# Optimization experiments

Hardware: AMD Instinct MI355X
Metric: run time of the kernel (lower is better)

The kernel has to match this reference:

```python
import jax, jax.numpy as jnp
import numpy as np

C1 = 0.01 ** 2
C2 = 0.03 ** 2
IN_CH = 3
WIN = 11
LEVELS = 5


def _gauss_kernel(k=WIN, sigma=1.5, c=IN_CH):
    ax = np.arange(k, dtype=np.float32) - (k - 1) / 2.0
    g = np.exp(-(ax ** 2) / (2.0 * sigma ** 2))
    g = g / g.sum()
    w2d = np.outer(g, g).astype(np.float32)  # [k,k]
    return jnp.asarray(np.tile(w2d[None, None], (c, 1, 1, 1)))  # [C,1,k,k]


def _dwconv(x, w):
    # depthwise (grouped) conv, 'same' padding for odd kernel
    pad = (w.shape[-1] - 1) // 2
    return jax.lax.conv_general_dilated(
        x, w, window_strides=(1, 1), padding=[(pad, pad), (pad, pad)],
        feature_group_count=x.shape[1],
        dimension_numbers=("NCHW", "OIHW", "NCHW"))


def _ssim_loss(i1, i2, w):
    m1 = _dwconv(i1, w)
    m2 = _dwconv(i2, w)
    m1sq = m1 * m1
    m2sq = m2 * m2
    m12 = m1 * m2
    s1 = _dwconv(i1 * i1, w) - m1sq
    s2 = _dwconv(i2 * i2, w) - m2sq
    s12 = _dwconv(i1 * i2, w) - m12
    ssim = (2 * m12 + C1) * (2 * s12 + C2) / ((m1sq + m2sq + C1) * (s1 + s2 + C2))
    return 1.0 - ssim.mean()


def _avg_pool2(x):
    B, C, H, W = x.shape
    return x.reshape(B, C, H // 2, 2, W // 2, 2).mean(axis=(3, 5))


def setup_inputs() -> dict:
    key = jax.random.key(0)
    k1, k2 = jax.random.split(key)
    img1 = jax.random.uniform(k1, (16, IN_CH, 512, 512), dtype=jnp.float32)
    img2 = jax.random.uniform(k2, (16, IN_CH, 512, 512), dtype=jnp.float32)
    inp = {"img1": img1, "img2": img2}
    for i in range(LEVELS):
        inp[f"g{i}"] = _gauss_kernel()
    return inp


def reference(img1, img2, g0, g1, g2, g3, g4):
    loss = jnp.asarray(0.0, dtype=img1.dtype)
    for w in (g0, g1, g2, g3, g4):
        loss = loss + _ssim_loss(img1, img2, w)
        img1 = _avg_pool2(img1)
        img2 = _avg_pool2(img2)
    return loss
```

## Files before the change

kernel.cpp:

```cpp
#include <hip/hip_runtime.h>
#include <math.h>

#define WIN 11
#define PAD 5
#define TW 64
#define TH 64

struct GW { float g[WIN]; };

template<bool EMIT>
__device__ __forceinline__ float ssim_wave_tile(
    const float* __restrict__ p1, const float* __restrict__ p2,
    int W, int X0, int Y0, const GW& gw, float2* __restrict__ rb,
    float* __restrict__ o1a, float* __restrict__ o1b, int Wout)
{
    const int lane = threadIdx.x & 63;
    const int gx = X0 + lane;
    const bool cval = gx < W;
    const int hx   = (lane < 5) ? (X0 - 5 + lane) : (X0 + 59 + lane);
    const bool hval = (lane < 10) && ((unsigned)hx < (unsigned)W);
    const int hpos = (lane < 5) ? lane : (64 + lane);
    const int cpos = 5 + lane;

    float vMp[11], vSp[11], vMq[11], vSq[11];
#pragma unroll
    for (int k = 0; k < 11; ++k) { vMp[k] = 0.f; vSp[k] = 0.f; vMq[k] = 0.f; vSq[k] = 0.f; }

    float part = 0.f;
    float pprev = 0.f, qprev = 0.f;
    float a, b, ah, bh;

    auto LOAD = [&](int t, float& oa, float& ob, float& oah, float& obh) {
        int y = Y0 - PAD + t;
        oa = 0.f; ob = 0.f; oah = 0.f; obh = 0.f;
        if ((unsigned)y < (unsigned)W) {
            const float* r1 = p1 + (size_t)y * W;
            const float* r2 = p2 + (size_t)y * W;
            if (cval) { oa  = r1[gx]; ob  = r2[gx]; }
            if (hval) { oah = r1[hx]; obh = r2[hx]; }
        }
    };

    LOAD(0, a, b, ah, bh);

#pragma unroll 2
    for (int t = 0; t < 74; ++t) {
        float na, nb, nah, nbh;
        LOAD(t + 1, na, nb, nah, nbh);

        float p = a + b, q = a - b;
        float ph = ah + bh, qh = ah - bh;
        rb[cpos] = make_float2(p, q);
        if (lane < 10) rb[hpos] = make_float2(ph, qh);
        __builtin_amdgcn_wave_barrier();

        float hp = 0.f, hq = 0.f, hpp = 0.f, hqq = 0.f;
#pragma unroll
        for (int j = 0; j < WIN; ++j) {
            float2 v = rb[lane + j];
            float g = gw.g[j];
            hp  = fmaf(g, v.x, hp);
            hpp = fmaf(g, v.x * v.x, hpp);
            hq  = fmaf(g, v.y, hq);
            hqq = fmaf(g, v.y * v.y, hqq);
        }
        __builtin_amdgcn_wave_barrier();

#pragma unroll
        for (int k = 0; k < 11; ++k) {
            float g = gw.g[10 - k];
            vMp[k] = fmaf(g, hp,  vMp[k]);
            vSp[k] = fmaf(g, hpp, vSp[k]);
            vMq[k] = fmaf(g, hq,  vMq[k]);
            vSq[k] = fmaf(g, hqq, vSq[k]);
        }

        if (EMIT) {
            if (t >= 6 && t <= 68 && (t & 1) == 0) {
                float sp_ = p + pprev, sq_ = q + qprev;
                float sp2 = sp_ + __shfl_down(sp_, 1, 64);
                float sq2 = sq_ + __shfl_down(sq_, 1, 64);
                if ((lane & 1) == 0) {
                    float P = sp2 * 0.25f, Q = sq2 * 0.25f;
                    int yo = (t - 6) >> 1;
                    size_t oo = (size_t)((Y0 >> 1) + yo) * Wout + ((X0 >> 1) + (lane >> 1));
                    o1a[oo] = (P + Q) * 0.5f;
                    o1b[oo] = (P - Q) * 0.5f;
                }
            }
            pprev = p; qprev = q;
        }

        if (t >= 10) {
            int o = t - 10;
            bool yok = (unsigned)(Y0 + o) < (unsigned)W;
            float Mp = vMp[0], Sp_ = vSp[0], Mq = vMq[0], Sq_ = vSq[0];
            const float C1v = 1e-4f, C2v = 9e-4f;
            float A = Mp * Mp, B = Mq * Mq;
            float ABp = A + B, ABm = A - B;
            float SSp = Sp_ + Sq_, SSm = Sp_ - Sq_;
            float n1 = fmaf(0.5f, ABm, C1v);
            float n2 = fmaf(0.5f, SSm - ABm, C2v);
            float e1 = fmaf(0.5f, ABp, C1v);
            float e2 = fmaf(0.5f, SSp - ABp, C2v);
            float v = (n1 * n2) * __builtin_amdgcn_rcpf(e1 * e2);
            part += (cval && yok) ? v : 0.f;
        }

#pragma unroll
        for (int k = 0; k < 10; ++k) {
            vMp[k] = vMp[k + 1]; vSp[k] = vSp[k + 1];
            vMq[k] = vMq[k + 1]; vSq[k] = vSq[k + 1];
        }
        vMp[10] = 0.f; vSp[10] = 0.f; vMq[10] = 0.f; vSq[10] = 0.f;

        a = na; b = nb; ah = nah; bh = nbh;
    }

    return part;
}

__global__ __launch_bounds__(256, 4) void ssim_l0_kernel(
    const float* __restrict__ i1, const float* __restrict__ i2,
    float* __restrict__ a1, float* __restrict__ b1,
    double* __restrict__ acc, GW gw)
{
    __shared__ float2 rbs[4][80];
    const int wid = threadIdx.x >> 6;
    const int w = blockIdx.x * 4 + wid;
    const int img = w >> 6;
    const int tt = w & 63;
    const int tx = tt & 7, ty = tt >> 3;
    const size_t off  = (size_t)img * 512 * 512;
    const size_t ooff = (size_t)img * 256 * 256;

    float part = ssim_wave_tile<true>(i1 + off, i2 + off, 512, tx * TW, ty * TH,
                                      gw, rbs[wid], a1 + ooff, b1 + ooff, 256);
#pragma unroll
    for (int o = 32; o > 0; o >>= 1) part += __shfl_down(part, o, 64);
    if ((threadIdx.x & 63) == 0) atomicAdd(acc, (double)part);
}

__global__ __launch_bounds__(256, 4) void ssim_rest_kernel(
    const float* __restrict__ a1, const float* __restrict__ b1,
    const float* __restrict__ a2, const float* __restrict__ b2,
    const float* __restrict__ a3, const float* __restrict__ b3,
    const float* __restrict__ a4, const float* __restrict__ b4,
    double* __restrict__ acc, GW gw)
{
    __shared__ float2 rbs[4][80];
    const int wid = threadIdx.x >> 6;
    const int w = blockIdx.x * 4 + wid;
    const int img = w / 22;
    const int r = w - img * 22;
    int lvl, tx, ty;
    if (r < 16)      { lvl = 1; tx = r & 3;        ty = r >> 2; }
    else if (r < 20) { lvl = 2; tx = (r - 16) & 1; ty = (r - 16) >> 1; }
    else if (r == 20){ lvl = 3; tx = 0; ty = 0; }
    else             { lvl = 4; tx = 0; ty = 0; }
    const int W = 512 >> lvl;
    const float* p1; const float* p2;
    switch (lvl) {
      case 1:  p1 = a1; p2 = b1; break;
      case 2:  p1 = a2; p2 = b2; break;
      case 3:  p1 = a3; p2 = b3; break;
      default: p1 = a4; p2 = b4; break;
    }
    const size_t off = (size_t)img * W * W;

    float part = ssim_wave_tile<false>(p1 + off, p2 + off, W, tx * TW, ty * TH,
                                       gw, rbs[wid], nullptr, nullptr, 0);
#pragma unroll
    for (int o = 32; o > 0; o >>= 1) part += __shfl_down(part, o, 64);
    if ((threadIdx.x & 63) == 0) atomicAdd(acc + lvl, (double)part);
}

__global__ __launch_bounds__(256) void pool_rest_kernel(
    const float* __restrict__ a1, const float* __restrict__ b1,
    float* __restrict__ a2, float* __restrict__ b2,
    float* __restrict__ a3, float* __restrict__ b3,
    float* __restrict__ a4, float* __restrict__ b4)
{
    __shared__ float l2[32][33];
    __shared__ float l3[16][17];
    const int tid = threadIdx.x;
    const int im = blockIdx.y;
    const int tb = blockIdx.x;
    const int tx = tb & 3, ty = tb >> 2;
    const bool second = im >= 48;
    const int ii = second ? im - 48 : im;
    const float* src = (second ? b1 : a1) + (size_t)ii * 256 * 256;
    float* o2 = (second ? b2 : a2) + (size_t)ii * 128 * 128;
    float* o3 = (second ? b3 : a3) + (size_t)ii * 64 * 64;
    float* o4 = (second ? b4 : a4) + (size_t)ii * 32 * 32;
    const int X0 = tx * 64, Y0 = ty * 64;

#pragma unroll
    for (int k = 0; k < 2; ++k) {
        int idx = tid + k * 256;
        int xp = idx & 15;
        int yo = idx >> 4;
        const float* rp = src + (size_t)(Y0 + 2 * yo) * 256 + (X0 + 4 * xp);
        float4 r0 = *(const float4*)rp;
        float4 r1 = *(const float4*)(rp + 256);
        float v0 = (r0.x + r0.y + r1.x + r1.y) * 0.25f;
        float v1 = (r0.z + r0.w + r1.z + r1.w) * 0.25f;
        l2[yo][2 * xp]     = v0;
        l2[yo][2 * xp + 1] = v1;
        float2* op = (float2*)(o2 + (size_t)((Y0 >> 1) + yo) * 128 + ((X0 >> 1) + 2 * xp));
        *op = make_float2(v0, v1);
    }
    __syncthreads();
    {
        int xo = tid & 15, yo = tid >> 4;
        if (yo < 16) {
            float v = (l2[2*yo][2*xo] + l2[2*yo][2*xo+1] +
                       l2[2*yo+1][2*xo] + l2[2*yo+1][2*xo+1]) * 0.25f;
            l3[yo][xo] = v;
            o3[(size_t)((Y0 >> 2) + yo) * 64 + ((X0 >> 2) + xo)] = v;
        }
    }
    __syncthreads();
    if (tid < 64) {
        int xo = tid & 7, yo = tid >> 3;
        float v = (l3[2*yo][2*xo] + l3[2*yo][2*xo+1] +
                   l3[2*yo+1][2*xo] + l3[2*yo+1][2*xo+1]) * 0.25f;
        o4[(size_t)((Y0 >> 3) + yo) * 32 + ((X0 >> 3) + xo)] = v;
    }
}

__global__ void final_kernel(const double* __restrict__ acc, float* __restrict__ out)
{
    double loss = 0.0;
#pragma unroll
    for (int l = 0; l < 5; ++l) {
        double cnt = 48.0 * (double)(512 >> l) * (double)(512 >> l);
        loss += 1.0 - acc[l] / cnt;
    }
    out[0] = (float)loss;
}

extern "C" void kernel_launch(void* const* d_in, const int* in_sizes, int n_in,
                              void* d_out, int out_size, void* d_ws, size_t ws_size,
                              hipStream_t stream)
{
    const float* img1 = (const float*)d_in[0];
    const float* img2 = (const float*)d_in[1];
    float* out = (float*)d_out;

    GW gw;
    double gs[WIN], sum = 0.0;
    for (int i = 0; i < WIN; ++i) {
        double ax = (double)i - 5.0;
        gs[i] = exp(-(ax * ax) / 4.5);
        sum += gs[i];
    }
    for (int i = 0; i < WIN; ++i) gw.g[i] = (float)(gs[i] / sum);

    double* acc = (double*)d_ws;
    float* base = (float*)((char*)d_ws + 64);
    const size_t n1 = 48ull * 256 * 256;
    const size_t n2 = 48ull * 128 * 128;
    const size_t n3 = 48ull * 64 * 64;
    const size_t n4 = 48ull * 32 * 32;
    float* a1 = base;      float* b1 = a1 + n1;
    float* a2 = b1 + n1;   float* b2 = a2 + n2;
    float* a3 = b2 + n2;   float* b3 = a3 + n3;
    float* a4 = b3 + n3;   float* b4 = a4 + n4;

    hipMemsetAsync(acc, 0, 5 * sizeof(double), stream);

    hipLaunchKernelGGL(ssim_l0_kernel, dim3(768), dim3(256), 0, stream,
                       img1, img2, a1, b1, acc, gw);

    hipLaunchKernelGGL(pool_rest_kernel, dim3(16, 96), dim3(256), 0, stream,
                       a1, b1, a2, b2, a3, b3, a4, b4);

    hipLaunchKernelGGL(ssim_rest_kernel, dim3(264), dim3(256), 0, stream,
                       a1, b1, a2, b2, a3, b3, a4, b4, acc, gw);

    hipLaunchKernelGGL(final_kernel, dim3(1), dim3(1), 0, stream, acc, out);
}
```

Baseline: 268.2 us.

## Use packed float2 FMAs and shorter row tiles for more waves

Rewrites the SSIM sliding-window math with 2-wide float vectors so the compiler can emit packed FMA instructions for the sum and difference channels together. The per-wave tile height is now a template parameter: 32 rows at level 0 and 16 rows at the coarser levels. This doubles the level-0 grid and roughly quadruples the rest-level grid, and launch bounds are raised to 6 blocks per CU. Shorter tiles add more vertical halo recomputation (10 extra rows per tile) in exchange for more parallelism and occupancy, and the tighter register budget could cause spills.

```diff
diff --git a/kernel.cpp b/kernel.cpp
--- a/kernel.cpp
+++ b/kernel.cpp
@@ -4,14 +4,15 @@
 #define WIN 11
 #define PAD 5
 #define TW 64
-#define TH 64
+
+typedef float v2f __attribute__((ext_vector_type(2)));
 
 struct GW { float g[WIN]; };
 
-template<bool EMIT>
+template<bool EMIT, int TH>
 __device__ __forceinline__ float ssim_wave_tile(
     const float* __restrict__ p1, const float* __restrict__ p2,
-    int W, int X0, int Y0, const GW& gw, float2* __restrict__ rb,
+    int W, int X0, int Y0, const GW& gw, v2f* __restrict__ rb,
     float* __restrict__ o1a, float* __restrict__ o1b, int Wout)
 {
     const int lane = threadIdx.x & 63;
@@ -22,12 +23,12 @@
     const int hpos = (lane < 5) ? lane : (64 + lane);
     const int cpos = 5 + lane;
 
-    float vMp[11], vSp[11], vMq[11], vSq[11];
-#pragma unroll
-    for (int k = 0; k < 11; ++k) { vMp[k] = 0.f; vSp[k] = 0.f; vMq[k] = 0.f; vSq[k] = 0.f; }
+    v2f vM[11], vS[11];
+#pragma unroll
+    for (int k = 0; k < 11; ++k) { vM[k] = (v2f){0.f, 0.f}; vS[k] = (v2f){0.f, 0.f}; }
 
     float part = 0.f;
-    float pprev = 0.f, qprev = 0.f;
+    v2f pqprev = {0.f, 0.f};
     float a, b, ah, bh;
 
     auto LOAD = [&](int t, float& oa, float& ob, float& oah, float& obh) {
@@ -44,42 +45,38 @@
     LOAD(0, a, b, ah, bh);
 
 #pragma unroll 2
-    for (int t = 0; t < 74; ++t) {
+    for (int t = 0; t < TH + 10; ++t) {
         float na, nb, nah, nbh;
         LOAD(t + 1, na, nb, nah, nbh);
 
-        float p = a + b, q = a - b;
-        float ph = ah + bh, qh = ah - bh;
-        rb[cpos] = make_float2(p, q);
-        if (lane < 10) rb[hpos] = make_float2(ph, qh);
+        v2f pq = { a + b, a - b };
+        v2f pqh = { ah + bh, ah - bh };
+        rb[cpos] = pq;
+        if (lane < 10) rb[hpos] = pqh;
         __builtin_amdgcn_wave_barrier();
 
-        float hp = 0.f, hq = 0.f, hpp = 0.f, hqq = 0.f;
+        v2f hM = {0.f, 0.f}, hS = {0.f, 0.f};
 #pragma unroll
         for (int j = 0; j < WIN; ++j) {
-            float2 v = rb[lane + j];
-            float g = gw.g[j];
-            hp  = fmaf(g, v.x, hp);
-            hpp = fmaf(g, v.x * v.x, hpp);
-            hq  = fmaf(g, v.y, hq);
-            hqq = fmaf(g, v.y * v.y, hqq);
+            v2f v = rb[lane + j];
+            v2f g = { gw.g[j], gw.g[j] };
+            hM = __builtin_elementwise_fma(g, v, hM);
+            hS = __builtin_elementwise_fma(g, v * v, hS);
         }
         __builtin_amdgcn_wave_barrier();
 
 #pragma unroll
         for (int k = 0; k < 11; ++k) {
-            float g = gw.g[10 - k];
-            vMp[k] = fmaf(g, hp,  vMp[k]);
-            vSp[k] = fmaf(g, hpp, vSp[k]);
-            vMq[k] = fmaf(g, hq,  vMq[k]);
-            vSq[k] = fmaf(g, hqq, vSq[k]);
+            v2f g = { gw.g[10 - k], gw.g[10 - k] };
+            vM[k] = __builtin_elementwise_fma(g, hM, vM[k]);
+            vS[k] = __builtin_elementwise_fma(g, hS, vS[k]);
         }
 
         if (EMIT) {
-            if (t >= 6 && t <= 68 && (t & 1) == 0) {
-                float sp_ = p + pprev, sq_ = q + qprev;
-                float sp2 = sp_ + __shfl_down(sp_, 1, 64);
-                float sq2 = sq_ + __shfl_down(sq_, 1, 64);
+            if (t >= 6 && t <= TH + 4 && (t & 1) == 0) {
+                v2f s = pq + pqprev;
+                float sp2 = s.x + __shfl_down(s.x, 1, 64);
+                float sq2 = s.y + __shfl_down(s.y, 1, 64);
                 if ((lane & 1) == 0) {
                     float P = sp2 * 0.25f, Q = sq2 * 0.25f;
                     int yo = (t - 6) >> 1;
@@ -88,13 +85,13 @@
                     o1b[oo] = (P - Q) * 0.5f;
                 }
             }
-            pprev = p; qprev = q;
+            pqprev = pq;
         }
 
         if (t >= 10) {
             int o = t - 10;
             bool yok = (unsigned)(Y0 + o) < (unsigned)W;
-            float Mp = vMp[0], Sp_ = vSp[0], Mq = vMq[0], Sq_ = vSq[0];
+            float Mp = vM[0].x, Mq = vM[0].y, Sp_ = vS[0].x, Sq_ = vS[0].y;
             const float C1v = 1e-4f, C2v = 9e-4f;
             float A = Mp * Mp, B = Mq * Mq;
             float ABp = A + B, ABm = A - B;
@@ -108,11 +105,8 @@
         }
 
 #pragma unroll
-        for (int k = 0; k < 10; ++k) {
-            vMp[k] = vMp[k + 1]; vSp[k] = vSp[k + 1];
-            vMq[k] = vMq[k + 1]; vSq[k] = vSq[k + 1];
-        }
-        vMp[10] = 0.f; vSp[10] = 0.f; vMq[10] = 0.f; vSq[10] = 0.f;
+        for (int k = 0; k < 10; ++k) { vM[k] = vM[k + 1]; vS[k] = vS[k + 1]; }
+        vM[10] = (v2f){0.f, 0.f}; vS[10] = (v2f){0.f, 0.f};
 
         a = na; b = nb; ah = nah; bh = nbh;
     }
@@ -120,44 +114,44 @@
     return part;
 }
 
-__global__ __launch_bounds__(256, 4) void ssim_l0_kernel(
+__global__ __launch_bounds__(256, 6) void ssim_l0_kernel(
     const float* __restrict__ i1, const float* __restrict__ i2,
     float* __restrict__ a1, float* __restrict__ b1,
     double* __restrict__ acc, GW gw)
 {
-    __shared__ float2 rbs[4][80];
+    __shared__ v2f rbs[4][80];
     const int wid = threadIdx.x >> 6;
     const int w = blockIdx.x * 4 + wid;
-    const int img = w >> 6;
-    const int tt = w & 63;
+    const int img = w >> 7;
+    const int tt = w & 127;
     const int tx = tt & 7, ty = tt >> 3;
     const size_t off  = (size_t)img * 512 * 512;
     const size_t ooff = (size_t)img * 256 * 256;
 
-    float part = ssim_wave_tile<true>(i1 + off, i2 + off, 512, tx * TW, ty * TH,
-                                      gw, rbs[wid], a1 + ooff, b1 + ooff, 256);
+    float part = ssim_wave_tile<true, 32>(i1 + off, i2 + off, 512, tx * 64, ty * 32,
+                                          gw, rbs[wid], a1 + ooff, b1 + ooff, 256);
 #pragma unroll
     for (int o = 32; o > 0; o >>= 1) part += __shfl_down(part, o, 64);
     if ((threadIdx.x & 63) == 0) atomicAdd(acc, (double)part);
 }
 
-__global__ __launch_bounds__(256, 4) void ssim_rest_kernel(
+__global__ __launch_bounds__(256, 6) void ssim_rest_kernel(
     const float* __restrict__ a1, const float* __restrict__ b1,
     const float* __restrict__ a2, const float* __restrict__ b2,
     const float* __restrict__ a3, const float* __restrict__ b3,
     const float* __restrict__ a4, const float* __restrict__ b4,
     double* __restrict__ acc, GW gw)
 {
-    __shared__ float2 rbs[4][80];
+    __shared__ v2f rbs[4][80];
     const int wid = threadIdx.x >> 6;
     const int w = blockIdx.x * 4 + wid;
-    const int img = w / 22;
-    const int r = w - img * 22;
+    const int img = w / 86;
+    const int r = w - img * 86;
     int lvl, tx, ty;
-    if (r < 16)      { lvl = 1; tx = r & 3;        ty = r >> 2; }
-    else if (r < 20) { lvl = 2; tx = (r - 16) & 1; ty = (r - 16) >> 1; }
-    else if (r == 20){ lvl = 3; tx = 0; ty = 0; }
-    else             { lvl = 4; tx = 0; ty = 0; }
+    if (r < 64)      { lvl = 1; tx = r & 3;  ty = r >> 2; }
+    else if (r < 80) { lvl = 2; int s = r - 64; tx = s & 1; ty = s >> 1; }
+    else if (r < 84) { lvl = 3; tx = 0; ty = r - 80; }
+    else             { lvl = 4; tx = 0; ty = r - 84; }
     const int W = 512 >> lvl;
     const float* p1; const float* p2;
     switch (lvl) {
@@ -168,8 +162,8 @@
     }
     const size_t off = (size_t)img * W * W;
 
-    float part = ssim_wave_tile<false>(p1 + off, p2 + off, W, tx * TW, ty * TH,
-                                       gw, rbs[wid], nullptr, nullptr, 0);
+    float part = ssim_wave_tile<false, 16>(p1 + off, p2 + off, W, tx * 64, ty * 16,
+                                           gw, rbs[wid], nullptr, nullptr, 0);
 #pragma unroll
     for (int o = 32; o > 0; o >>= 1) part += __shfl_down(part, o, 64);
     if ((threadIdx.x & 63) == 0) atomicAdd(acc + lvl, (double)part);
@@ -270,13 +264,13 @@
 
     hipMemsetAsync(acc, 0, 5 * sizeof(double), stream);
 
-    hipLaunchKernelGGL(ssim_l0_kernel, dim3(768), dim3(256), 0, stream,
+    hipLaunchKernelGGL(ssim_l0_kernel, dim3(1536), dim3(256), 0, stream,
                        img1, img2, a1, b1, acc, gw);
 
     hipLaunchKernelGGL(pool_rest_kernel, dim3(16, 96), dim3(256), 0, stream,
                        a1, b1, a2, b2, a3, b3, a4, b4);
 
-    hipLaunchKernelGGL(ssim_rest_kernel, dim3(264), dim3(256), 0, stream,
+    hipLaunchKernelGGL(ssim_rest_kernel, dim3(1032), dim3(256), 0, stream,
                        a1, b1, a2, b2, a3, b3, a4, b4, acc, gw);
 
     hipLaunchKernelGGL(final_kernel, dim3(1), dim3(1), 0, stream, acc, out);
```

New measurement: 449.6 us. +67.7%, slower.
